# Kernel optimization log

Measured on AMD Instinct MI355X. Metric: run time of the kernel, lower is better.

The kernel has to match this reference:

```python
import jax, jax.numpy as jnp
import numpy as np

M, K, N, G = 64, 4096, 11008, 128  # tokens, infeatures, outfeatures, group_size
NUM_GROUPS = K // G  # 32


def _fp8_round_trip(w):
    # Simulate FP8 E4M3 storage of the quantized weight codes.
    return w.astype(jnp.float8_e4m3fn).astype(jnp.float32)


def setup_inputs() -> dict:
    key = jax.random.key(0)
    k1, k2, k3, k4 = jax.random.split(key, 4)
    x = jax.random.normal(k1, (M, K), dtype=jnp.float32)
    # FP8-representable weight codes (post round-trip, stored as f32 values)
    weight = _fp8_round_trip(jax.random.normal(k2, (N, K), dtype=jnp.float32) * 2.0)
    # Per-(out_feature, group) dequant scales, strictly positive
    weight_scale = jax.random.uniform(k3, (N, NUM_GROUPS), dtype=jnp.float32,
                                      minval=0.005, maxval=0.02)
    bias = jax.random.normal(k4, (N,), dtype=jnp.float32)
    return {"x": x, "weight": weight, "weight_scale": weight_scale, "bias": bias}


def reference(x, weight, weight_scale, bias):
    # Dequantize: each group of `G` consecutive in-features of an output row
    # shares one scale -> w_deq[o, i] = weight[o, i] * scale[o, i // G]
    n, k = weight.shape
    g = k // weight_scale.shape[1]
    w_deq = (weight.reshape(n, -1, g) * weight_scale[:, :, None]).reshape(n, k)
    # Fused dequant-matmul: out[m, o] = sum_i x[m, i] * w_deq[o, i] + bias[o]
    out = jnp.einsum("mk,nk->mn", x, w_deq) + bias
    return out
```

## Files before the change

### kernel.cpp

```cpp
#include <hip/hip_runtime.h>


#define Md 64
#define Kd 4096
#define Nd 11008
#define NGROUPS 32
#define BN 64
#define KSPLIT 8
#define KCHUNK (Kd / KSPLIT)
#define NSTAGE (KCHUNK / 64)
#define NGRP (KCHUNK / 128)
#define KBC (KCHUNK / 32)

typedef __attribute__((ext_vector_type(8))) __bf16 bf16x8;
typedef __attribute__((ext_vector_type(4))) float f32x4;

__global__ __launch_bounds__(256)
void prep(const float* __restrict__ x, __bf16* __restrict__ xf,
          const float* __restrict__ bias, float* __restrict__ out)
{
    if (blockIdx.x < 128) {
        const int tid  = blockIdx.x * 256 + threadIdx.x;
        const int lane = tid & 63;
        const int t    = (tid >> 6) & 3;
        const int kb   = tid >> 8;
        const int row  = t * 16 + (lane & 15);
        const int col  = kb * 32 + (lane >> 4) * 8;
        const float4 a = *(const float4*)(x + (size_t)row * Kd + col);
        const float4 b = *(const float4*)(x + (size_t)row * Kd + col + 4);
        bf16x8 v = {(__bf16)a.x, (__bf16)a.y, (__bf16)a.z, (__bf16)a.w,
                    (__bf16)b.x, (__bf16)b.y, (__bf16)b.z, (__bf16)b.w};
        *(bf16x8*)(xf + (size_t)tid * 8) = v;
    } else {
        const int i4 = (blockIdx.x - 128) * 256 + threadIdx.x;
        const int n  = (i4 * 4) % Nd;
        *(float4*)(out + (size_t)i4 * 4) = *(const float4*)(bias + n);
    }
}

__global__ __launch_bounds__(256, 4)
void qlinear_pass1(const float* __restrict__ w,
                   const __bf16* __restrict__ xf,
                   const float* __restrict__ scale,
                   float* __restrict__ out)
{
    const int tid  = threadIdx.x;
    const int wv   = tid >> 6;
    const int lane = tid & 63;
    const int quad = lane >> 4;
    const int ln   = lane & 15;

    const int n0 = blockIdx.x * BN;
    const int ky = blockIdx.y;
    const int k0 = ky * KCHUNK;

    __shared__ alignas(16) float lds_w[2][BN * 64];

    const float* src[4];
    #pragma unroll
    for (int j = 0; j < 4; ++j) {
        const int r   = wv * 16 + j * 4 + quad;
        const int c16 = ln ^ (r & 7);
        src[j] = w + (size_t)(n0 + r) * Kd + k0 + c16 * 4;
    }

    const __bf16* xp = xf + (size_t)ky * KBC * 4 * 512 + (size_t)lane * 8;

    const int nrow = n0 + wv * 16 + ln;
    float4 sc4 = *(const float4*)(scale + (size_t)nrow * NGROUPS + ky * NGRP);
    const float sc[4] = {sc4.x, sc4.y, sc4.z, sc4.w};

    const int rr = wv * 16 + ln;
    const int rx = rr & 7;

    f32x4 acc[4];
    #pragma unroll
    for (int t = 0; t < 4; ++t) acc[t] = (f32x4){0.f, 0.f, 0.f, 0.f};

    #pragma unroll
    for (int j = 0; j < 4; ++j)
        __builtin_amdgcn_global_load_lds(
            (const __attribute__((address_space(1))) void*)src[j],
            (__attribute__((address_space(3))) void*)&lds_w[0][(wv * 4 + j) * 256],
            16, 0, 0);
    __syncthreads();

    #pragma unroll
    for (int g = 0; g < NGRP; ++g) {
        f32x4 pg[4];
        #pragma unroll
        for (int t = 0; t < 4; ++t) pg[t] = (f32x4){0.f, 0.f, 0.f, 0.f};

        #pragma unroll
        for (int half = 0; half < 2; ++half) {
            const int s   = g * 2 + half;
            const int buf = s & 1;

            if (s + 1 < NSTAGE) {
                #pragma unroll
                for (int j = 0; j < 4; ++j)
                    __builtin_amdgcn_global_load_lds(
                        (const __attribute__((address_space(1))) void*)(src[j] + (s + 1) * 64),
                        (__attribute__((address_space(3))) void*)&lds_w[buf ^ 1][(wv * 4 + j) * 256],
                        16, 0, 0);
            }

            #pragma unroll
            for (int ks = 0; ks < 2; ++ks) {
                const int kb = s * 2 + ks;
                bf16x8 xv[4];
                #pragma unroll
                for (int t = 0; t < 4; ++t)
                    xv[t] = *(const bf16x8*)(xp + ((size_t)kb * 4 + t) * 512);

                const int c0 = ks * 8 + quad * 2;
                f32x4 fa = *(const f32x4*)&lds_w[buf][rr * 64 + (((c0    ) ^ rx) << 2)];
                f32x4 fb = *(const f32x4*)&lds_w[buf][rr * 64 + (((c0 + 1) ^ rx) << 2)];
                bf16x8 wf = {(__bf16)fa.x, (__bf16)fa.y, (__bf16)fa.z, (__bf16)fa.w,
                             (__bf16)fb.x, (__bf16)fb.y, (__bf16)fb.z, (__bf16)fb.w};
                #pragma unroll
                for (int t = 0; t < 4; ++t)
                    pg[t] = __builtin_amdgcn_mfma_f32_16x16x32_bf16(xv[t], wf, pg[t],
                                                                    0, 0, 0);
            }
            __syncthreads();
        }

        const float s = sc[g];
        #pragma unroll
        for (int t = 0; t < 4; ++t)
            #pragma unroll
            for (int r = 0; r < 4; ++r)
                acc[t][r] += s * pg[t][r];
    }

    float* op = out + n0 + wv * 16 + ln;
    #pragma unroll
    for (int t = 0; t < 4; ++t)
        #pragma unroll
        for (int r = 0; r < 4; ++r)
            unsafeAtomicAdd(&op[(size_t)(t * 16 + quad * 4 + r) * Nd], acc[t][r]);
}

extern "C" void kernel_launch(void* const* d_in, const int* in_sizes, int n_in,
                              void* d_out, int out_size, void* d_ws, size_t ws_size,
                              hipStream_t stream) {
    const float* x     = (const float*)d_in[0];
    const float* w     = (const float*)d_in[1];
    const float* scale = (const float*)d_in[2];
    const float* bias  = (const float*)d_in[3];
    float* out = (float*)d_out;
    float* ws  = (float*)d_ws;

    __bf16* xf = (__bf16*)ws;

    prep<<<816, 256, 0, stream>>>(x, xf, bias, out);

    dim3 grid1(Nd / BN, KSPLIT);
    qlinear_pass1<<<grid1, 256, 0, stream>>>(w, xf, scale, out);
}
```

Baseline: 269.2 us.

## Deepen weight prefetch to 4-buffer ring with distance-2 and vmcnt waits

Splits each 64-wide K stage into 32-wide stages held in a 4-deep LDS ring, issuing async global-to-LDS loads two stages ahead. __syncthreads is replaced by explicit s_waitcnt vmcnt plus s_barrier, so loads still in flight are not drained at every step. The goal is more overlap of weight streaming with MFMA work, at the cost of more barriers per K and reliance on hand-counted vmcnt values that the x global loads could also affect.

```diff
diff --git a/kernel.cpp b/kernel.cpp
--- a/kernel.cpp
+++ b/kernel.cpp
@@ -8,7 +8,7 @@
 #define BN 64
 #define KSPLIT 8
 #define KCHUNK (Kd / KSPLIT)
-#define NSTAGE (KCHUNK / 64)
+#define NST (KCHUNK / 32)
 #define NGRP (KCHUNK / 128)
 #define KBC (KCHUNK / 32)
 
@@ -54,15 +54,25 @@
     const int ky = blockIdx.y;
     const int k0 = ky * KCHUNK;
 
-    __shared__ alignas(16) float lds_w[2][BN * 64];
+    __shared__ alignas(16) float lds_w[4][BN * 32];
 
-    const float* src[4];
+    const float* src[2];
     #pragma unroll
-    for (int j = 0; j < 4; ++j) {
-        const int r   = wv * 16 + j * 4 + quad;
-        const int c16 = ln ^ (r & 7);
+    for (int j = 0; j < 2; ++j) {
+        const int r   = wv * 16 + j * 8 + (lane >> 3);
+        const int c16 = (lane & 7) ^ (r & 7);
         src[j] = w + (size_t)(n0 + r) * Kd + k0 + c16 * 4;
     }
+
+#define STAGE(S, B)                                                            \
+    do {                                                                       \
+        _Pragma("unroll")                                                      \
+        for (int j = 0; j < 2; ++j)                                            \
+            __builtin_amdgcn_global_load_lds(                                  \
+                (const __attribute__((address_space(1))) void*)(src[j] + (S) * 32), \
+                (__attribute__((address_space(3))) void*)&lds_w[B][(wv * 16 + j * 8) * 32], \
+                16, 0, 0);                                                     \
+    } while (0)
 
     const __bf16* xp = xf + (size_t)ky * KBC * 4 * 512 + (size_t)lane * 8;
 
@@ -77,13 +87,10 @@
     #pragma unroll
     for (int t = 0; t < 4; ++t) acc[t] = (f32x4){0.f, 0.f, 0.f, 0.f};
 
-    #pragma unroll
-    for (int j = 0; j < 4; ++j)
-        __builtin_amdgcn_global_load_lds(
-            (const __attribute__((address_space(1))) void*)src[j],
-            (__attribute__((address_space(3))) void*)&lds_w[0][(wv * 4 + j) * 256],
-            16, 0, 0);
-    __syncthreads();
+    STAGE(0, 0);
+    STAGE(1, 1);
+    asm volatile("s_waitcnt vmcnt(2)" ::: "memory");
+    __builtin_amdgcn_s_barrier();
 
     #pragma unroll
     for (int g = 0; g < NGRP; ++g) {
@@ -92,38 +99,36 @@
         for (int t = 0; t < 4; ++t) pg[t] = (f32x4){0.f, 0.f, 0.f, 0.f};
 
         #pragma unroll
-        for (int half = 0; half < 2; ++half) {
-            const int s   = g * 2 + half;
-            const int buf = s & 1;
+        for (int sub = 0; sub < 4; ++sub) {
+            const int s   = g * 4 + sub;
+            const int buf = s & 3;
 
-            if (s + 1 < NSTAGE) {
-                #pragma unroll
-                for (int j = 0; j < 4; ++j)
-                    __builtin_amdgcn_global_load_lds(
-                        (const __attribute__((address_space(1))) void*)(src[j] + (s + 1) * 64),
-                        (__attribute__((address_space(3))) void*)&lds_w[buf ^ 1][(wv * 4 + j) * 256],
-                        16, 0, 0);
-            }
+            if (s + 2 < NST) STAGE(s + 2, (s + 2) & 3);
+
+            bf16x8 xv[4];
+            #pragma unroll
+            for (int t = 0; t < 4; ++t)
+                xv[t] = *(const bf16x8*)(xp + ((size_t)s * 4 + t) * 512);
+
+            const int cA = (quad * 2) ^ rx;
+            const int cB = (quad * 2 + 1) ^ rx;
+            f32x4 fa = *(const f32x4*)&lds_w[buf][rr * 32 + cA * 4];
+            f32x4 fb = *(const f32x4*)&lds_w[buf][rr * 32 + cB * 4];
+            bf16x8 wf = {(__bf16)fa.x, (__bf16)fa.y, (__bf16)fa.z, (__bf16)fa.w,
+                         (__bf16)fb.x, (__bf16)fb.y, (__bf16)fb.z, (__bf16)fb.w};
 
             #pragma unroll
-            for (int ks = 0; ks < 2; ++ks) {
-                const int kb = s * 2 + ks;
-                bf16x8 xv[4];
-                #pragma unroll
-                for (int t = 0; t < 4; ++t)
-                    xv[t] = *(const bf16x8*)(xp + ((size_t)kb * 4 + t) * 512);
+            for (int t = 0; t < 4; ++t)
+                pg[t] = __builtin_amdgcn_mfma_f32_16x16x32_bf16(xv[t], wf, pg[t],
+                                                                0, 0, 0);
 
-                const int c0 = ks * 8 + quad * 2;
-                f32x4 fa = *(const f32x4*)&lds_w[buf][rr * 64 + (((c0    ) ^ rx) << 2)];
-                f32x4 fb = *(const f32x4*)&lds_w[buf][rr * 64 + (((c0 + 1) ^ rx) << 2)];
-                bf16x8 wf = {(__bf16)fa.x, (__bf16)fa.y, (__bf16)fa.z, (__bf16)fa.w,
-                             (__bf16)fb.x, (__bf16)fb.y, (__bf16)fb.z, (__bf16)fb.w};
-                #pragma unroll
-                for (int t = 0; t < 4; ++t)
-                    pg[t] = __builtin_amdgcn_mfma_f32_16x16x32_bf16(xv[t], wf, pg[t],
-                                                                    0, 0, 0);
+            if (s + 1 < NST) {
+                if (s + 2 < NST)
+                    asm volatile("s_waitcnt vmcnt(2)" ::: "memory");
+                else
+                    asm volatile("s_waitcnt vmcnt(0)" ::: "memory");
+                __builtin_amdgcn_s_barrier();
             }
-            __syncthreads();
         }
 
         const float s = sc[g];
@@ -140,6 +145,7 @@
         #pragma unroll
         for (int r = 0; r < 4; ++r)
             unsafeAtomicAdd(&op[(size_t)(t * 16 + quad * 4 + r) * Nd], acc[t][r]);
+#undef STAGE
 }
 
 extern "C" void kernel_launch(void* const* d_in, const int* in_sizes, int n_in,
```

After: 276.9 us. +2.9%, slower.
